# Performance work log

Hardware: AMD Instinct MI355X
Metric: run time of the kernel (lower is better)

Reference implementation:

```python
import math
import jax, jax.numpy as jnp
from jax import lax
import numpy as np

B, DIM, H, W = 8, 256, 64, 64
D_STATE, D_CONV, EXPAND = 16, 4, 2
D_INNER = EXPAND * DIM
DT_RANK = math.ceil(DIM / 16)
POS_LEN = 16
EPS = 1e-5
GN_GROUPS = 32


def setup_inputs() -> dict:
    key = jax.random.key(0)
    ks = iter(jax.random.split(key, 24))
    rn = lambda shape, s=0.02: jax.random.normal(next(ks), shape, jnp.float32) * s
    inp = {}
    inp["x"] = jax.random.normal(next(ks), (B, DIM, H, W), jnp.float32)
    inp["pos_emb"] = rn((1, DIM, POS_LEN), 1.0)
    inp["ln_g"] = jnp.ones((DIM,), jnp.float32)
    inp["ln_b"] = jnp.zeros((DIM,), jnp.float32)
    inp["m_in_w"] = rn((2, 2 * D_INNER, DIM))
    inp["m_conv_w"] = rn((2, D_INNER, D_CONV), 0.1)
    inp["m_conv_b"] = jnp.zeros((2, D_INNER), jnp.float32)
    inp["m_xproj_w"] = rn((2, DT_RANK + 2 * D_STATE, D_INNER))
    inp["m_dt_w"] = rn((2, D_INNER, DT_RANK), 0.1)
    inp["m_dt_b"] = rn((2, D_INNER), 0.1)
    inp["m_A_log"] = jnp.tile(jnp.log(jnp.arange(1, D_STATE + 1, dtype=jnp.float32))[None, None, :], (2, D_INNER, 1))
    inp["m_D"] = jnp.ones((2, D_INNER), jnp.float32)
    inp["m_out_w"] = rn((2, DIM, D_INNER))
    inp["proj_w"] = rn((DIM, 2 * DIM))
    inp["proj_b"] = jnp.zeros((DIM,), jnp.float32)
    inp["up_dw_w"] = rn((DIM, 1, 3, 3), 0.1)
    inp["up_bn1_g"] = jnp.ones((DIM,), jnp.float32)
    inp["up_bn1_b"] = jnp.zeros((DIM,), jnp.float32)
    inp["up_pw_w"] = rn((DIM, DIM), 0.05)
    inp["up_bn2_g"] = jnp.ones((DIM,), jnp.float32)
    inp["up_bn2_b"] = jnp.zeros((DIM,), jnp.float32)
    inp["down_pw_w"] = rn((DIM, DIM), 0.05)
    inp["down_bn_g"] = jnp.ones((DIM,), jnp.float32)
    inp["down_bn_b"] = jnp.zeros((DIM,), jnp.float32)
    inp["gn_g"] = jnp.ones((DIM,), jnp.float32)
    inp["gn_b"] = jnp.zeros((DIM,), jnp.float32)
    return inp


def reference(x, pos_emb, ln_g, ln_b, m_in_w, m_conv_w, m_conv_b, m_xproj_w, m_dt_w, m_dt_b,
              m_A_log, m_D, m_out_w, proj_w, proj_b, up_dw_w, up_bn1_g, up_bn1_b, up_pw_w,
              up_bn2_g, up_bn2_b, down_pw_w, down_bn_g, down_bn_b, gn_g, gn_b):
    Bx, C, Hh, Ww = x.shape

    def ln(t):  # LayerNorm over last dim (shared self.norm)
        m = jnp.mean(t, -1, keepdims=True)
        v = jnp.mean((t - m) ** 2, -1, keepdims=True)
        return (t - m) * lax.rsqrt(v + EPS) * ln_g + ln_b

    def bn(t, g, b):  # BatchNorm2d in eval mode with default running stats (mean 0, var 1)
        return t * (g / jnp.sqrt(1.0 + EPS))[None, :, None, None] + b[None, :, None, None]

    def gn(t):  # GroupNorm(32, C), shared params (self.bn)
        Bn, Cn, Hn, Wn = t.shape
        tg = t.reshape(Bn, GN_GROUPS, Cn // GN_GROUPS, Hn, Wn)
        m = jnp.mean(tg, (2, 3, 4), keepdims=True)
        v = jnp.mean((tg - m) ** 2, (2, 3, 4), keepdims=True)
        tg = (tg - m) * lax.rsqrt(v + EPS)
        return tg.reshape(Bn, Cn, Hn, Wn) * gn_g[None, :, None, None] + gn_b[None, :, None, None]

    def interp_pos(N):  # F.interpolate(pos_embed, size=N, mode='linear', align_corners=False)
        coords = jnp.maximum((jnp.arange(N, dtype=jnp.float32) + 0.5) * (POS_LEN / N) - 0.5, 0.0)
        i0 = jnp.floor(coords).astype(jnp.int32)
        i1 = jnp.minimum(i0 + 1, POS_LEN - 1)
        wgt = coords - i0.astype(jnp.float32)
        return pos_emb[:, :, i0] * (1.0 - wgt) + pos_emb[:, :, i1] * wgt  # (1,C,N)

    def pe_branch(vals, idx, N):  # vals (B,C,N); indices interp at same size = identity
        t = vals + interp_pos(N) + idx.astype(jnp.float32)
        return ln(jnp.swapaxes(t, 1, 2))  # (B,N,C)

    def mamba(u, d):  # standard mamba_ssm selective scan; u (B,L,C)
        xz = jnp.einsum('blc,ic->bli', u, m_in_w[d])
        xh, zg = jnp.split(xz, 2, -1)
        xc = lax.conv_general_dilated(jnp.swapaxes(xh, 1, 2), m_conv_w[d][:, None, :], (1,),
                                      [(D_CONV - 1, 0)], feature_group_count=D_INNER,
                                      dimension_numbers=('NCH', 'OIH', 'NCH'))
        xc = jnp.swapaxes(jax.nn.silu(xc + m_conv_b[d][None, :, None]), 1, 2)  # (B,L,di)
        dbl = jnp.einsum('bld,ed->ble', xc, m_xproj_w[d])
        dt = dbl[..., :DT_RANK]
        Bm = dbl[..., DT_RANK:DT_RANK + D_STATE]
        Cm = dbl[..., DT_RANK + D_STATE:]
        dt = jax.nn.softplus(jnp.einsum('blr,dr->bld', dt, m_dt_w[d]) + m_dt_b[d])  # (B,L,di)
        A = -jnp.exp(m_A_log[d])  # (di,ds)
        dA = jnp.exp(dt[..., None] * A)  # (B,L,di,ds)
        dBx = dt[..., None] * Bm[:, :, None, :] * xc[..., None]

        def step(h, inps):
            dA_t, dBx_t, C_t = inps
            h = dA_t * h + dBx_t
            return h, jnp.einsum('bds,bs->bd', h, C_t)

        h0 = jnp.zeros((u.shape[0], D_INNER, D_STATE), u.dtype)
        _, ys = lax.scan(step, h0, (jnp.swapaxes(dA, 0, 1), jnp.swapaxes(dBx, 0, 1), jnp.swapaxes(Cm, 0, 1)))
        y = jnp.swapaxes(ys, 0, 1) + xc * m_D[d]
        y = y * jax.nn.silu(zg)
        return jnp.einsum('bld,od->blo', y, m_out_w[d])

    # z branch: depthwise ConvTranspose2d(k3,s2,p1,op1) + BN + ReLU + pw conv + BN, then ReLU6
    z = lax.conv_general_dilated(x, jnp.flip(up_dw_w, (2, 3)), (1, 1), [(1, 2), (1, 2)],
                                 lhs_dilation=(2, 2), feature_group_count=C,
                                 dimension_numbers=('NCHW', 'OIHW', 'NCHW'))  # (B,C,2H,2W)
    z = jax.nn.relu(bn(z, up_bn1_g, up_bn1_b))
    z = jnp.einsum('bchw,oc->bohw', z, up_pw_w)
    z = jnp.clip(bn(z, up_bn2_g, up_bn2_b), 0.0, 6.0)

    col_max = pe_branch(jnp.max(x, 2), jnp.argmax(x, 2), Ww)
    col_min = pe_branch(jnp.min(x, 2), jnp.argmin(x, 2), Ww)
    row_max = pe_branch(jnp.max(x, 3), jnp.argmax(x, 3), Hh)
    row_min = pe_branch(jnp.min(x, 3), jnp.argmin(x, 3), Hh)
    result_max = jnp.concatenate([col_max, row_max], 1)  # (B, W+H, C)
    result_min = jnp.concatenate([col_min, row_min], 1)

    fm_max = ln(mamba(result_max, 0))
    fm_min = ln(mamba(result_min, 0))
    bm_max = ln(mamba(jnp.flip(result_max, 1), 1))
    bm_min = ln(mamba(jnp.flip(result_min, 1), 1))

    res_max = jnp.concatenate([fm_max, jnp.flip(bm_max, 1)], -1) @ proj_w.T + proj_b
    res_min = jnp.concatenate([fm_min, jnp.flip(bm_min, 1)], -1) @ proj_w.T + proj_b
    res_max = ln(res_max)[:, :, None, :]  # (B,L,1,C)
    res_min = ln(res_min)[:, None, :, :]  # (B,1,L,C)

    res = jnp.transpose(res_max + res_min, (0, 3, 1, 2))  # (B,C,L,L), L=H+W=2H
    res = jnp.clip(res + 3.0, 0.0, 6.0) / 6.0 * z  # h_sigmoid gate
    res = gn(res)
    res = jnp.einsum('bchw,oc->bohw', res[:, :, ::2, ::2], down_pw_w)  # pw conv stride 2
    res = bn(res, down_bn_g, down_bn_b)
    res = gn(res)
    res = res + x
    res = gn(res)
    return res
```

## Files before the change

kernel.cpp:

```cpp
#include <hip/hip_runtime.h>
#include <hip/hip_bf16.h>
#include <math.h>

typedef __hip_bfloat16 bf16;
typedef __attribute__((ext_vector_type(8))) short short8_t;
typedef __attribute__((ext_vector_type(4))) short short4_t;
typedef __attribute__((ext_vector_type(4))) float f32x4_t;

#define EPSV 1e-5f
#define BNSC 0.99999500003749968f

__device__ __forceinline__ float bf2f(bf16 v){ return __bfloat162float(v); }
__device__ __forceinline__ bf16 f2bf(float v){ return __float2bfloat16(v); }

__device__ __forceinline__ float blk_sum(float v, float* sm){
  int tid = threadIdx.x;
  #pragma unroll
  for(int o=32;o>0;o>>=1) v += __shfl_down(v, o, 64);
  if((tid&63)==0) sm[tid>>6] = v;
  __syncthreads();
  float s = 0.f;
  int nw = blockDim.x>>6;
  for(int i=0;i<nw;i++) s += sm[i];
  __syncthreads();
  return s;
}

__device__ __forceinline__ float softplusf(float x){
  return (x > 20.f) ? x : __logf(1.f + __expf(x));
}
__device__ __forceinline__ float siluf(float x){
  return x / (1.f + __expf(-x));
}

__global__ void prep_weights(const float* __restrict__ in_w, const float* __restrict__ out_w,
                             const float* __restrict__ pw_w, const float* __restrict__ dpw_w,
                             const float* __restrict__ proj_w,
                             bf16* __restrict__ Winb, bf16* __restrict__ Woutb,
                             bf16* __restrict__ Wub, bf16* __restrict__ Wdb,
                             float* __restrict__ PT, float* __restrict__ gacc){
  int idx = blockIdx.x*256 + threadIdx.x;
  if(idx < 1536) gacc[idx] = 0.f;
  if(idx < 524288){ Winb[idx] = f2bf(in_w[idx]); return; }
  if(idx < 786432){ int i=idx-524288; Woutb[i] = f2bf(out_w[i]); return; }
  if(idx < 851968){ int i=idx-786432; Wub[i] = f2bf(pw_w[i]); return; }
  if(idx < 917504){ int i=idx-851968; Wdb[i] = f2bf(dpw_w[i]); return; }
  int k = idx - 917504;
  int i = k >> 9, j = k & 511;
  PT[j*256 + i] = proj_w[k];
}

__global__ void r1_reduce_pe(const float* __restrict__ x, const float* __restrict__ pe,
                             float* __restrict__ pmax, float* __restrict__ pmin){
  __shared__ float tile[64*65];
  int bc = blockIdx.x;
  int b = bc >> 8, c = bc & 255;
  const float* xp = x + ((size_t)bc << 12);
  for(int i=threadIdx.x; i<4096; i+=64)
    tile[(i>>6)*65 + (i&63)] = xp[i];
  __syncthreads();
  int t = threadIdx.x;
  float cmx=-3.4e38f, cmn=3.4e38f; int cax=0, can=0;
  for(int h=0;h<64;h++){
    float v = tile[h*65 + t];
    if(v > cmx){ cmx=v; cax=h; }
    if(v < cmn){ cmn=v; can=h; }
  }
  float rmx=-3.4e38f, rmn=3.4e38f; int rax=0, ran=0;
  for(int w=0;w<64;w++){
    float v = tile[t*65 + w];
    if(v > rmx){ rmx=v; rax=w; }
    if(v < rmn){ rmn=v; ran=w; }
  }
  float coords = fmaxf((t + 0.5f)*0.25f - 0.5f, 0.f);
  int i0 = (int)floorf(coords);
  int i1 = min(i0+1, 15);
  float wg = coords - (float)i0;
  float pos = pe[c*16+i0]*(1.f-wg) + pe[c*16+i1]*wg;
  size_t base_col = ((size_t)b*128 + t)*256 + c;
  size_t base_row = ((size_t)b*128 + 64 + t)*256 + c;
  pmax[base_col] = cmx + pos + (float)cax;
  pmin[base_col] = cmn + pos + (float)can;
  pmax[base_row] = rmx + pos + (float)rax;
  pmin[base_row] = rmn + pos + (float)ran;
}

__global__ void ln_rows2(float* __restrict__ bufA, float* __restrict__ bufB,
                         const float* __restrict__ g, const float* __restrict__ bb,
                         bf16* __restrict__ boutA, bf16* __restrict__ boutB){
  __shared__ float sm[8];
  int row = blockIdx.x, t = threadIdx.x;
  float* buf; bf16* bout;
  if(row < 1024){ buf = bufA; bout = boutA; }
  else { buf = bufB; bout = boutB; row -= 1024; }
  float v = buf[(size_t)row*256 + t];
  float m = blk_sum(v, sm) * (1.f/256.f);
  float dv = v - m;
  float var = blk_sum(dv*dv, sm) * (1.f/256.f);
  float r = dv * rsqrtf(var + EPSV) * g[t] + bb[t];
  buf[(size_t)row*256 + t] = r;
  if(bout) bout[(size_t)row*256 + t] = f2bf(r);
}

__global__ __launch_bounds__(256,2)
void m1_mfma(const bf16* __restrict__ ubmax, const bf16* __restrict__ ubmin,
             const bf16* __restrict__ Win, float* __restrict__ xz){
  __shared__ bf16 att[64*264];
  int bx = blockIdx.x;
  int it = bx & 3, lt = (bx>>2)&1, b = (bx>>3)&7, r = bx>>6;
  int d = r & 1;
  const bf16* u = (r < 2) ? ubmax : ubmin;
  int flip = r & 1;
  int t = threadIdx.x;
  {
    int pr = t>>5, cc = (t&31)*8;
    #pragma unroll
    for(int i=0;i<8;i++){
      int p = pr + i*8;
      int l = lt*64 + p;
      int le = flip ? (127 - l) : l;
      short8_t v = *(const short8_t*)((const short*)u + ((size_t)(b*128 + le))*256 + cc);
      *(short8_t*)&att[p*264 + cc] = v;
    }
  }
  __syncthreads();
  int wv = t>>6, lane = t&63, quad = lane>>4, l16 = lane&15;
  int m0 = wv*64;
  f32x4_t acc[4][4];
  #pragma unroll
  for(int ms=0;ms<4;ms++)
    #pragma unroll
    for(int ns=0;ns<4;ns++) acc[ms][ns] = (f32x4_t){0.f,0.f,0.f,0.f};
  const short* wbase = (const short*)Win + ((size_t)d*1024 + it*256)*256;
  for(int k0=0;k0<256;k0+=32){
    short8_t afr[4], bfr[4];
    #pragma unroll
    for(int ms=0;ms<4;ms++)
      afr[ms] = *(const short8_t*)(wbase + (size_t)(m0 + ms*16 + l16)*256 + k0 + quad*8);
    #pragma unroll
    for(int ns=0;ns<4;ns++)
      bfr[ns] = *(const short8_t*)&att[(ns*16 + l16)*264 + k0 + quad*8];
    #pragma unroll
    for(int ms=0;ms<4;ms++)
      #pragma unroll
      for(int ns=0;ns<4;ns++)
        acc[ms][ns] = __builtin_amdgcn_mfma_f32_16x16x32_bf16(afr[ms], bfr[ns], acc[ms][ns], 0,0,0);
  }
  int rb = r*8 + b;
  #pragma unroll
  for(int ns=0;ns<4;ns++){
    int l = lt*64 + ns*16 + l16;
    float* dst = xz + ((size_t)rb*128 + l)*1024 + it*256;
    #pragma unroll
    for(int ms=0;ms<4;ms++){
      int i = m0 + ms*16 + quad*4;
      *(f32x4_t*)(dst + i) = acc[ms][ns];
    }
  }
}

__global__ __launch_bounds__(256)
void m234(const float* __restrict__ xz, const float* __restrict__ cw,
          const float* __restrict__ cb, const float* __restrict__ xproj,
          const float* __restrict__ dtw, const float* __restrict__ dtbias,
          float* __restrict__ xc, float* __restrict__ dbl, float* __restrict__ dt){
  __shared__ float xzs[4*512];
  __shared__ float xcs[512];
  __shared__ float pbuf[192];
  __shared__ float dblrow[48];
  int rowid = blockIdx.x;
  int rb = rowid >> 7, l = rowid & 127;
  int d = (rb >> 3) & 1;
  int t = threadIdx.x;
  #pragma unroll
  for(int i=0;i<8;i++){
    int idx = t + i*256;
    int r = idx >> 9, dd = idx & 511;
    int ls = l - 3 + r;
    xzs[idx] = (ls >= 0) ? xz[((size_t)rb*128 + ls)*1024 + dd] : 0.f;
  }
  __syncthreads();
  #pragma unroll
  for(int i=0;i<2;i++){
    int dd = t + i*256;
    const float* w = cw + (size_t)(d*512 + dd)*4;
    float s = cb[d*512 + dd];
    #pragma unroll
    for(int k=0;k<4;k++) s += xzs[k*512 + dd] * w[k];
    s = siluf(s);
    xcs[dd] = s;
    xc[(size_t)rowid*512 + dd] = s;
  }
  __syncthreads();
  if(t < 192){
    int e = t >> 2, part = t & 3;
    const float* wp = xproj + (size_t)(d*48 + e)*512 + part*128;
    const float* xr = xcs + part*128;
    float s = 0.f;
    for(int k=0;k<128;k++) s += xr[k]*wp[k];
    pbuf[t] = s;
  }
  __syncthreads();
  if(t < 48){
    float s = pbuf[t*4] + pbuf[t*4+1] + pbuf[t*4+2] + pbuf[t*4+3];
    dblrow[t] = s;
    dbl[(size_t)rowid*48 + t] = s;
  }
  __syncthreads();
  #pragma unroll
  for(int i=0;i<2;i++){
    int dd = t + i*256;
    const float* wp = dtw + (size_t)(d*512 + dd)*16;
    float s = dtbias[d*512 + dd];
    #pragma unroll
    for(int r=0;r<16;r++) s += dblrow[r]*wp[r];
    dt[(size_t)rowid*512 + dd] = softplusf(s);
  }
}

__global__ void m5_passA(const float* __restrict__ dt, const float* __restrict__ xc,
                         const float* __restrict__ dbl, const float* __restrict__ Alog,
                         float* __restrict__ P, float* __restrict__ Hl){
  int bx = blockIdx.x;
  int seg = bx & 7, half = (bx>>3)&1, rb = bx>>4;
  int dd = half*256 + threadIdx.x;
  int d = (rb>>3)&1;
  float A[16], h[16], pr[16];
  #pragma unroll
  for(int s=0;s<16;s++){
    A[s] = -__expf(Alog[(size_t)(d*512 + dd)*16 + s]);
    h[s] = 0.f; pr[s] = 1.f;
  }
  int l0 = seg*16;
  for(int l=l0;l<l0+16;l++){
    size_t row = (size_t)rb*128 + l;
    float dtv = dt[row*512 + dd];
    float xcv = xc[row*512 + dd];
    float bx_ = dtv*xcv;
    const float* dr = dbl + row*48;
    #pragma unroll
    for(int s=0;s<16;s++){
      float dA = __expf(dtv*A[s]);
      pr[s] *= dA;
      h[s] = dA*h[s] + bx_*dr[16+s];
    }
  }
  size_t o = ((size_t)(rb*8 + seg)*512 + dd)*16;
  #pragma unroll
  for(int s=0;s<16;s+=4){
    *(f32x4_t*)(P  + o + s) = (f32x4_t){pr[s],pr[s+1],pr[s+2],pr[s+3]};
    *(f32x4_t*)(Hl + o + s) = (f32x4_t){h[s],h[s+1],h[s+2],h[s+3]};
  }
}

__global__ void m5_passB(const float* __restrict__ dt, const float* __restrict__ xc,
                         const float* __restrict__ dbl, const float* __restrict__ xz,
                         const float* __restrict__ Alog, const float* __restrict__ Dp,
                         const float* __restrict__ P, const float* __restrict__ Hl,
                         bf16* __restrict__ ybb){
  int bx = blockIdx.x;
  int seg = bx & 7, half = (bx>>3)&1, rb = bx>>4;
  int dd = half*256 + threadIdx.x;
  int d = (rb>>3)&1;
  float A[16], h[16];
  #pragma unroll
  for(int s=0;s<16;s++){
    A[s] = -__expf(Alog[(size_t)(d*512 + dd)*16 + s]);
    h[s] = 0.f;
  }
  for(int j=0;j<seg;j++){
    size_t o = ((size_t)(rb*8 + j)*512 + dd)*16;
    #pragma unroll
    for(int s=0;s<16;s+=4){
      f32x4_t pv = *(const f32x4_t*)(P + o + s);
      f32x4_t hv = *(const f32x4_t*)(Hl + o + s);
      h[s]   = pv[0]*h[s]   + hv[0];
      h[s+1] = pv[1]*h[s+1] + hv[1];
      h[s+2] = pv[2]*h[s+2] + hv[2];
      h[s+3] = pv[3]*h[s+3] + hv[3];
    }
  }
  float Dv = Dp[d*512 + dd];
  int l0 = seg*16;
  for(int l=l0;l<l0+16;l++){
    size_t row = (size_t)rb*128 + l;
    float dtv = dt[row*512 + dd];
    float xcv = xc[row*512 + dd];
    float zgv = xz[row*1024 + 512 + dd];
    const float* dr = dbl + row*48;
    float bx_ = dtv*xcv;
    float y = 0.f;
    #pragma unroll
    for(int s=0;s<16;s++){
      h[s] = __expf(dtv*A[s])*h[s] + bx_*dr[16+s];
      y += h[s]*dr[32+s];
    }
    ybb[row*512 + dd] = f2bf((y + xcv*Dv) * siluf(zgv));
  }
}

__global__ __launch_bounds__(256,2)
void m6_mfma(const bf16* __restrict__ ybb, const bf16* __restrict__ Wout,
             const float* __restrict__ lng, const float* __restrict__ lnb,
             float* __restrict__ mo){
  __shared__ char smem[64*264*4];
  bf16* ybt = (bf16*)smem;
  float* fbuf = (float*)smem;
  int bx = blockIdx.x;
  int lt = bx & 1, b = (bx>>1)&7, r = bx>>4;
  int d = r & 1, rb = r*8 + b;
  size_t rowbase = (size_t)rb*128 + lt*64;
  int t = threadIdx.x;
  for(int i=t;i<4096;i+=256){
    int row = i>>6, c8 = (i&63)*8;
    short8_t v = *(const short8_t*)((const short*)ybb + (rowbase + row)*512 + c8);
    *(short8_t*)&ybt[row*520 + c8] = v;
  }
  __syncthreads();
  int wv = t>>6, lane = t&63, quad = lane>>4, l16 = lane&15;
  int m0 = wv*64;
  f32x4_t acc[4][4];
  #pragma unroll
  for(int ms=0;ms<4;ms++)
    #pragma unroll
    for(int ns=0;ns<4;ns++) acc[ms][ns] = (f32x4_t){0.f,0.f,0.f,0.f};
  const short* wbase = (const short*)Wout + (size_t)d*256*512;
  for(int k0=0;k0<512;k0+=32){
    short8_t afr[4], bfr[4];
    #pragma unroll
    for(int ms=0;ms<4;ms++)
      afr[ms] = *(const short8_t*)(wbase + (size_t)(m0 + ms*16 + l16)*512 + k0 + quad*8);
    #pragma unroll
    for(int ns=0;ns<4;ns++)
      bfr[ns] = *(const short8_t*)&ybt[(ns*16 + l16)*520 + k0 + quad*8];
    #pragma unroll
    for(int ms=0;ms<4;ms++)
      #pragma unroll
      for(int ns=0;ns<4;ns++)
        acc[ms][ns] = __builtin_amdgcn_mfma_f32_16x16x32_bf16(afr[ms], bfr[ns], acc[ms][ns], 0,0,0);
  }
  __syncthreads();
  #pragma unroll
  for(int ns=0;ns<4;ns++){
    int row = ns*16 + l16;
    #pragma unroll
    for(int ms=0;ms<4;ms++){
      int o = m0 + ms*16 + quad*4;
      *(f32x4_t*)(fbuf + row*264 + o) = acc[ms][ns];
    }
  }
  __syncthreads();
  {
    int row = t >> 2, part = t & 3;
    const float* fr = fbuf + row*264;
    float s = 0.f;
    #pragma unroll 8
    for(int j=0;j<64;j++){
      int col = part*64 + ((j + part*16) & 63);
      s += fr[col];
    }
    s += __shfl_xor(s, 1, 64);
    s += __shfl_xor(s, 2, 64);
    float m = s * (1.f/256.f);
    float q = 0.f;
    #pragma unroll 8
    for(int j=0;j<64;j++){
      int col = part*64 + ((j + part*16) & 63);
      float dv = fr[col] - m;
      q += dv*dv;
    }
    q += __shfl_xor(q, 1, 64);
    q += __shfl_xor(q, 2, 64);
    float rs = rsqrtf(q*(1.f/256.f) + EPSV);
    float* dst = mo + (rowbase + row)*256;
    for(int j=0;j<64;j++){
      int col = part*64 + j;
      dst[col] = (fr[col] - m)*rs*lng[col] + lnb[col];
    }
  }
}

__global__ void m7_proj(const float* __restrict__ mo, const float* __restrict__ PT,
                        const float* __restrict__ pb, const float* __restrict__ lng,
                        const float* __restrict__ lnb, float* __restrict__ resm,
                        float* __restrict__ resn){
  __shared__ float ct[16*512];
  __shared__ float fbuf[16*264];
  int bx = blockIdx.x;
  int tt = bx >> 6, rem = bx & 63, b = rem >> 3, lt = rem & 7;
  int fr_ = tt*2, br = tt*2 + 1;
  for(int i=threadIdx.x;i<16*512;i+=256){
    int lr = i >> 9, k = i & 511;
    int l = lt*16 + lr;
    ct[i] = (k < 256)
      ? mo[(((size_t)(fr_*8+b)*128) + l)*256 + k]
      : mo[(((size_t)(br*8+b)*128) + (127-l))*256 + (k-256)];
  }
  __syncthreads();
  float acc[16];
  #pragma unroll
  for(int q=0;q<16;q++) acc[q] = 0.f;
  int t = threadIdx.x;
  for(int k=0;k<512;k++){
    float pv = PT[(size_t)k*256 + t];
    #pragma unroll
    for(int q=0;q<16;q++) acc[q] += pv * ct[(q<<9) + k];
  }
  float bias = pb[t];
  #pragma unroll
  for(int q=0;q<16;q++) fbuf[q*264 + t] = acc[q] + bias;
  __syncthreads();
  float* dstbuf = tt ? resn : resm;
  if(t < 64){
    int row = t >> 2, part = t & 3;
    const float* fr = fbuf + row*264;
    float s = 0.f;
    for(int j=0;j<64;j++){
      int col = part*64 + ((j + part*16) & 63);
      s += fr[col];
    }
    s += __shfl_xor(s, 1, 64);
    s += __shfl_xor(s, 2, 64);
    float m = s * (1.f/256.f);
    float q = 0.f;
    for(int j=0;j<64;j++){
      int col = part*64 + ((j + part*16) & 63);
      float dv = fr[col] - m;
      q += dv*dv;
    }
    q += __shfl_xor(q, 1, 64);
    q += __shfl_xor(q, 2, 64);
    float rs = rsqrtf(q*(1.f/256.f) + EPSV);
    float* dst = dstbuf + ((size_t)b*128 + lt*16 + row)*256;
    for(int j=0;j<64;j++){
      int col = part*64 + j;
      dst[col] = (fr[col] - m)*rs*lng[col] + lnb[col];
    }
  }
}

__global__ __launch_bounds__(256)
void k1_deconv_T(const float* __restrict__ x, const float* __restrict__ wdw,
                 const float* __restrict__ g1, const float* __restrict__ b1,
                 bf16* __restrict__ zT){
  __shared__ float in[2*64*33];
  __shared__ bf16 ot[64*80];
  int bx = blockIdx.x;
  int cb = bx & 3, half = (bx>>2)&1, h = (bx>>3)&127, b = bx>>10;
  int c0 = cb*64, w0 = half*64, iw0 = w0>>1;
  int h_odd = h & 1;
  int ihA = h_odd ? (h-1)>>1 : h>>1;
  int ihB = (h+1)>>1;
  bool hasB = h_odd && (ihB < 64);
  for(int i = threadIdx.x; i < 4224; i += 256){
    int row = i / 2112;
    int rem = i - row*2112;
    int c = rem / 33;
    int iw = rem - c*33;
    int ihl = row ? ihB : ihA;
    bool valid = (iw0 + iw < 64) && (row == 0 || hasB);
    in[i] = valid ? x[(((size_t)b*256 + c0 + c)<<12) + (ihl<<6) + iw0 + iw] : 0.f;
  }
  __syncthreads();
  int c = threadIdx.x & 63, g = threadIdx.x >> 6;
  const float* wp = wdw + (c0+c)*9;
  int khA3 = h_odd ? 6 : 3;
  float wA0 = wp[khA3], wA1 = wp[khA3+1], wA2 = wp[khA3+2];
  float wB0 = wp[0],    wB1 = wp[1],      wB2 = wp[2];
  float scale = g1[c0+c]*BNSC, bias = b1[c0+c];
  const float* inA = in + c*33;
  const float* inB = in + 2112 + c*33;
  #pragma unroll
  for(int i=0;i<16;i++){
    int wi = g*16 + i;
    float s;
    if(!(i&1)){
      int iw = wi>>1;
      s = inA[iw]*wA1 + inB[iw]*wB1;
    } else {
      int iwa = (wi-1)>>1, iwb = (wi+1)>>1;
      s = inA[iwa]*wA2 + inA[iwb]*wA0 + inB[iwa]*wB2 + inB[iwb]*wB0;
    }
    ot[wi*80 + c] = f2bf(fmaxf(s*scale + bias, 0.f));
  }
  __syncthreads();
  int rr = threadIdx.x >> 3;
  int co = (threadIdx.x & 7) * 8;
  size_t obase = (((size_t)b*16384) + (size_t)h*128 + w0)*256 + c0;
  #pragma unroll
  for(int pass=0; pass<2; pass++){
    int wi = rr + pass*32;
    short8_t v = *(const short8_t*)&ot[wi*80 + co];
    *(short8_t*)((short*)zT + obase + (size_t)wi*256 + co) = v;
  }
}

__global__ __launch_bounds__(256,2)
void k2_mfma(const bf16* __restrict__ zT, const bf16* __restrict__ Wub,
             const float* __restrict__ g2, const float* __restrict__ b2,
             const float* __restrict__ resm, const float* __restrict__ resn,
             bf16* __restrict__ resT, float* __restrict__ gsum, float* __restrict__ gssq){
  __shared__ bf16 zt[128*264];
  __shared__ float lsum[32], lssq[32];
  int b = blockIdx.y;
  int p0 = blockIdx.x*128;
  int t = threadIdx.x;
  if(t < 32){ lsum[t] = 0.f; lssq[t] = 0.f; }
  {
    const short* src = (const short*)zT + (((size_t)b*16384 + p0)*256);
    int pr = t>>5;
    int cc = (t&31)*8;
    #pragma unroll
    for(int i=0;i<16;i++){
      int p = pr + i*8;
      short8_t v = *(const short8_t*)(src + (size_t)p*256 + cc);
      *(short8_t*)&zt[p*264 + cc] = v;
    }
  }
  __syncthreads();
  int wv = t>>6, lane = t&63, quad = lane>>4, l16 = lane&15;
  int m0 = wv*64;
  f32x4_t acc[4][8];
  #pragma unroll
  for(int ms=0;ms<4;ms++)
    #pragma unroll
    for(int ns=0;ns<8;ns++) acc[ms][ns] = (f32x4_t){0.f,0.f,0.f,0.f};
  const short* wp = (const short*)Wub + (size_t)(m0 + l16)*256 + quad*8;
  short8_t afr[4];
  #pragma unroll
  for(int ms=0;ms<4;ms++) afr[ms] = *(const short8_t*)(wp + (size_t)ms*16*256);
  for(int k0=0;k0<256;k0+=32){
    short8_t anext[4];
    if(k0 + 32 < 256){
      #pragma unroll
      for(int ms=0;ms<4;ms++)
        anext[ms] = *(const short8_t*)(wp + (size_t)ms*16*256 + k0 + 32);
    }
    short8_t bfr[8];
    #pragma unroll
    for(int ns=0;ns<8;ns++)
      bfr[ns] = *(const short8_t*)&zt[(ns*16 + l16)*264 + k0 + quad*8];
    #pragma unroll
    for(int ms=0;ms<4;ms++)
      #pragma unroll
      for(int ns=0;ns<8;ns++)
        acc[ms][ns] = __builtin_amdgcn_mfma_f32_16x16x32_bf16(afr[ms], bfr[ns], acc[ms][ns], 0,0,0);
    #pragma unroll
    for(int ms=0;ms<4;ms++) afr[ms] = anext[ms];
  }
  float sm_[4] = {0.f,0.f,0.f,0.f}, sq_[4] = {0.f,0.f,0.f,0.f};
  #pragma unroll
  for(int ns=0;ns<8;ns++){
    int p = p0 + ns*16 + l16;
    int hh = p>>7, ww = p&127;
    const float* rm = resm + ((size_t)b*128+hh)*256;
    const float* rn = resn + ((size_t)b*128+ww)*256;
    size_t orow = ((size_t)b*16384 + p)*256;
    #pragma unroll
    for(int ms=0;ms<4;ms++){
      int o = m0 + ms*16 + quad*4;
      f32x4_t a = acc[ms][ns];
      f32x4_t gv = *(const f32x4_t*)(g2+o);
      f32x4_t bv = *(const f32x4_t*)(b2+o);
      f32x4_t rmv = *(const f32x4_t*)(rm+o);
      f32x4_t rnv = *(const f32x4_t*)(rn+o);
      alignas(8) bf16 ov[4];
      #pragma unroll
      for(int r=0;r<4;r++){
        float zv = a[r]*(gv[r]*BNSC) + bv[r];
        zv = fminf(fmaxf(zv, 0.f), 6.f);
        float gate = fminf(fmaxf(rmv[r]+rnv[r]+3.f, 0.f), 6.f)*(1.f/6.f);
        float val = zv*gate;
        sm_[ms] += val;
        sq_[ms] += val*val;
        ov[r] = f2bf(val);
      }
      *(short4_t*)((short*)resT + orow + o) = *(const short4_t*)ov;
    }
  }
  #pragma unroll
  for(int ms=0;ms<4;ms++){
    int g = ((m0 + ms*16) >> 3) + (quad >> 1);
    atomicAdd(&lsum[g], sm_[ms]);
    atomicAdd(&lssq[g], sq_[ms]);
  }
  __syncthreads();
  if(t < 32){
    atomicAdd(&gsum[b*32 + t], lsum[t]);
    atomicAdd(&gssq[b*32 + t], lssq[t]);
  }
}

__global__ __launch_bounds__(256,2)
void k4_mfma(const bf16* __restrict__ resT, const bf16* __restrict__ Wdb,
             const float* __restrict__ gsum1, const float* __restrict__ gssq1,
             const float* __restrict__ gng, const float* __restrict__ gnb,
             const float* __restrict__ dbg, const float* __restrict__ dbb,
             float* __restrict__ t1, float* __restrict__ gsum2, float* __restrict__ gssq2){
  __shared__ bf16 at[64*264];
  __shared__ float sc[256], sb[256];
  __shared__ float stm[32], str[32];
  __shared__ float l2s[32], l2q[32];
  int b = blockIdx.y;
  int q0 = blockIdx.x*64;
  int t = threadIdx.x;
  if(t < 32){
    l2s[t] = 0.f; l2q[t] = 0.f;
    float m = gsum1[b*32+t] * (1.f/131072.f);
    float var = gssq1[b*32+t] * (1.f/131072.f) - m*m;
    stm[t] = m;
    str[t] = rsqrtf(var + EPSV);
  }
  __syncthreads();
  {
    int cch = t, g = cch>>3;
    float m = stm[g], rs = str[g];
    float s = rs*gng[cch];
    sc[cch] = s; sb[cch] = gnb[cch] - m*s;
  }
  __syncthreads();
  {
    int pr = t>>5;
    int cc = (t&31)*8;
    #pragma unroll
    for(int i=0;i<8;i++){
      int q = pr + i*8;
      int qq = q0 + q;
      int y = qq>>6, xw = qq&63;
      size_t srow = ((size_t)b*16384 + (size_t)y*256 + xw*2)*256;
      short8_t v = *(const short8_t*)((const short*)resT + srow + cc);
      const bf16* vv = (const bf16*)&v;
      alignas(16) bf16 ov[8];
      #pragma unroll
      for(int j=0;j<8;j++) ov[j] = f2bf(bf2f(vv[j])*sc[cc+j] + sb[cc+j]);
      *(short8_t*)&at[q*264 + cc] = *(const short8_t*)ov;
    }
  }
  __syncthreads();
  int wv = t>>6, lane = t&63, quad = lane>>4, l16 = lane&15;
  int n0 = wv*64;
  f32x4_t acc[4][4];
  #pragma unroll
  for(int ms=0;ms<4;ms++)
    #pragma unroll
    for(int ns=0;ns<4;ns++) acc[ms][ns] = (f32x4_t){0.f,0.f,0.f,0.f};
  for(int k0=0;k0<256;k0+=32){
    short8_t afr[4], bfr[4];
    #pragma unroll
    for(int ms=0;ms<4;ms++) afr[ms] = *(const short8_t*)&at[(ms*16 + l16)*264 + k0 + quad*8];
    const short* wp = (const short*)Wdb + (size_t)(n0 + l16)*256 + k0 + quad*8;
    #pragma unroll
    for(int ns=0;ns<4;ns++) bfr[ns] = *(const short8_t*)(wp + (size_t)ns*16*256);
    #pragma unroll
    for(int ms=0;ms<4;ms++)
      #pragma unroll
      for(int ns=0;ns<4;ns++)
        acc[ms][ns] = __builtin_amdgcn_mfma_f32_16x16x32_bf16(afr[ms], bfr[ns], acc[ms][ns], 0,0,0);
  }
  #pragma unroll
  for(int ns=0;ns<4;ns++){
    int o = n0 + ns*16 + l16;
    float s2 = dbg[o]*BNSC, bb2 = dbb[o];
    float* dst = t1 + (((size_t)b*256 + o) << 12);
    float s_=0.f, q_=0.f;
    #pragma unroll
    for(int ms=0;ms<4;ms++){
      int ps = q0 + ms*16 + quad*4;
      f32x4_t a = acc[ms][ns];
      f32x4_t ov;
      #pragma unroll
      for(int r=0;r<4;r++){
        ov[r] = a[r]*s2 + bb2;
        s_ += ov[r];
        q_ += ov[r]*ov[r];
      }
      *(f32x4_t*)(dst + ps) = ov;
    }
    atomicAdd(&l2s[o>>3], s_);
    atomicAdd(&l2q[o>>3], q_);
  }
  __syncthreads();
  if(t < 32){
    atomicAdd(&gsum2[b*32 + t], l2s[t]);
    atomicAdd(&gssq2[b*32 + t], l2q[t]);
  }
}

__global__ void k6_gn_add(float* __restrict__ t1, const float* __restrict__ x,
                          const float* __restrict__ gsum2, const float* __restrict__ gssq2,
                          const float* __restrict__ gng, const float* __restrict__ gnb,
                          float* __restrict__ gsum3, float* __restrict__ gssq3){
  __shared__ float sm[8];
  int i4 = blockIdx.x*256 + threadIdx.x;
  int idx = i4 << 2;
  int c = (idx >> 12) & 255, b = idx >> 20, g = c >> 3;
  float m2 = gsum2[b*32+g] * (1.f/32768.f);
  float var = gssq2[b*32+g] * (1.f/32768.f) - m2*m2;
  float rs = rsqrtf(var + EPSV);
  float scl = rs*gng[c], off = gnb[c] - m2*scl;
  f32x4_t tv = *(const f32x4_t*)(t1 + idx);
  f32x4_t xv = *(const f32x4_t*)(x + idx);
  f32x4_t ov;
  float S = 0.f, Q = 0.f;
  #pragma unroll
  for(int r=0;r<4;r++){
    float v = tv[r]*scl + off + xv[r];
    ov[r] = v;
    S += v; Q += v*v;
  }
  *(f32x4_t*)(t1 + idx) = ov;
  S = blk_sum(S, sm);
  Q = blk_sum(Q, sm);
  if(threadIdx.x == 0){
    atomicAdd(&gsum3[b*32 + g], S);
    atomicAdd(&gssq3[b*32 + g], Q);
  }
}

__global__ void k8_gn_out(const float* __restrict__ t1, const float* __restrict__ gsum3,
                          const float* __restrict__ gssq3, const float* __restrict__ gng,
                          const float* __restrict__ gnb, float* __restrict__ out){
  int i4 = blockIdx.x*256 + threadIdx.x;
  int idx = i4 << 2;
  int c = (idx >> 12) & 255, b = idx >> 20, g = c >> 3;
  float m = gsum3[b*32+g] * (1.f/32768.f);
  float var = gssq3[b*32+g] * (1.f/32768.f) - m*m;
  float rs = rsqrtf(var + EPSV);
  float scl = rs*gng[c], off = gnb[c] - m*scl;
  f32x4_t tv = *(const f32x4_t*)(t1 + idx);
  f32x4_t ov;
  #pragma unroll
  for(int r=0;r<4;r++) ov[r] = tv[r]*scl + off;
  *(f32x4_t*)(out + idx) = ov;
}

extern "C" void kernel_launch(void* const* d_in, const int* in_sizes, int n_in,
                              void* d_out, int out_size, void* d_ws, size_t ws_size,
                              hipStream_t stream){
  const float* x      = (const float*)d_in[0];
  const float* pos    = (const float*)d_in[1];
  const float* ln_g   = (const float*)d_in[2];
  const float* ln_b   = (const float*)d_in[3];
  const float* in_w   = (const float*)d_in[4];
  const float* conv_w = (const float*)d_in[5];
  const float* conv_b = (const float*)d_in[6];
  const float* xproj  = (const float*)d_in[7];
  const float* dt_w   = (const float*)d_in[8];
  const float* dt_b   = (const float*)d_in[9];
  const float* A_log  = (const float*)d_in[10];
  const float* Dp     = (const float*)d_in[11];
  const float* out_w  = (const float*)d_in[12];
  const float* proj_w = (const float*)d_in[13];
  const float* proj_b = (const float*)d_in[14];
  const float* dw_w   = (const float*)d_in[15];
  const float* bn1g   = (const float*)d_in[16];
  const float* bn1b   = (const float*)d_in[17];
  const float* pw_w   = (const float*)d_in[18];
  const float* bn2g   = (const float*)d_in[19];
  const float* bn2b   = (const float*)d_in[20];
  const float* dpw_w  = (const float*)d_in[21];
  const float* dbng   = (const float*)d_in[22];
  const float* dbnb   = (const float*)d_in[23];
  const float* gng    = (const float*)d_in[24];
  const float* gnb    = (const float*)d_in[25];
  float* out = (float*)d_out;

  float* ws = (float*)d_ws;
  bf16*  resT = (bf16*)ws;
  bf16*  zT   = (bf16*)(ws + 16777216);
  float* scanP = ws + 16777216;
  float* scanH = ws + 16777216 + 2097152;
  float* zone = ws + 33554432;
  float* xz   = zone;
  float* xc   = xz  + 4194304;
  float* dbl  = xc  + 2097152;
  float* dtb  = dbl + 196608;
  bf16*  ybb  = (bf16*)(dtb + 2097152);
  float* t1   = zone;
  float* mo   = zone + 9633792;
  float* resm = mo   + 1048576;
  float* resn = resm + 262144;
  float* pmax = resn + 262144;
  float* pmin = pmax + 262144;
  float* PT   = pmin + 262144;
  bf16*  ubmax= (bf16*)(PT + 131072);
  bf16*  ubmin= (bf16*)(PT + 131072 + 131072);
  bf16*  Winb = (bf16*)(PT + 131072 + 262144);
  bf16*  Woutb= (bf16*)(PT + 131072 + 524288);
  bf16*  Wub  = (bf16*)(PT + 131072 + 655360);
  bf16*  Wdb  = (bf16*)(PT + 131072 + 688128);
  float* gacc = PT + 131072 + 720896;
  float* gsum1 = gacc,        *gssq1 = gacc + 256;
  float* gsum2 = gacc + 512,  *gssq2 = gacc + 768;
  float* gsum3 = gacc + 1024, *gssq3 = gacc + 1280;

  prep_weights<<<4096,256,0,stream>>>(in_w, out_w, pw_w, dpw_w, proj_w,
                                      Winb, Woutb, Wub, Wdb, PT, gacc);

  r1_reduce_pe<<<2048,64,0,stream>>>(x, pos, pmax, pmin);
  ln_rows2<<<2048,256,0,stream>>>(pmax, pmin, ln_g, ln_b, ubmax, ubmin);

  m1_mfma<<<256,256,0,stream>>>(ubmax, ubmin, Winb, xz);
  m234<<<4096,256,0,stream>>>(xz, conv_w, conv_b, xproj, dt_w, dt_b, xc, dbl, dtb);
  m5_passA<<<512,256,0,stream>>>(dtb, xc, dbl, A_log, scanP, scanH);
  m5_passB<<<512,256,0,stream>>>(dtb, xc, dbl, xz, A_log, Dp, scanP, scanH, ybb);
  m6_mfma<<<64,256,0,stream>>>(ybb, Woutb, ln_g, ln_b, mo);
  m7_proj<<<128,256,0,stream>>>(mo, PT, proj_b, ln_g, ln_b, resm, resn);

  k1_deconv_T<<<8192,256,0,stream>>>(x, dw_w, bn1g, bn1b, zT);
  k2_mfma<<<dim3(128,8),256,0,stream>>>(zT, Wub, bn2g, bn2b, resm, resn,
                                        resT, gsum1, gssq1);

  k4_mfma<<<dim3(64,8),256,0,stream>>>(resT, Wdb, gsum1, gssq1,
                                       gng, gnb, dbng, dbnb, t1, gsum2, gssq2);

  k6_gn_add<<<8192,256,0,stream>>>(t1, x, gsum2, gssq2, gng, gnb, gsum3, gssq3);
  k8_gn_out<<<8192,256,0,stream>>>(t1, gsum3, gssq3, gng, gnb, out);
}
```

Before: 527.1 us.

## Enlarge k4 tile, prefetch weights, replace LDS atomics with wave shuffle reductions

In k2 and k4 the group-norm statistics are now summed with cross-lane shuffles and written to global memory with direct atomics, which removes the shared-memory atomics and a block barrier. k4 now processes 128 output positions per block instead of 64, which halves the grid and reuses each loaded weight fragment across twice as many MFMAs. It also prefetches the next k-step's weight fragments into registers. The larger accumulator array raises register pressure and the larger LDS tile can lower occupancy, and the global atomics now come from more threads.

Result: slower. 553.1 us (+4.9%).

```diff
diff --git a/kernel.cpp b/kernel.cpp
--- a/kernel.cpp
+++ b/kernel.cpp
@@ -501,11 +501,9 @@
              const float* __restrict__ resm, const float* __restrict__ resn,
              bf16* __restrict__ resT, float* __restrict__ gsum, float* __restrict__ gssq){
   __shared__ bf16 zt[128*264];
-  __shared__ float lsum[32], lssq[32];
   int b = blockIdx.y;
   int p0 = blockIdx.x*128;
   int t = threadIdx.x;
-  if(t < 32){ lsum[t] = 0.f; lssq[t] = 0.f; }
   {
     const short* src = (const short*)zT + (((size_t)b*16384 + p0)*256);
     int pr = t>>5;
@@ -580,14 +578,17 @@
   }
   #pragma unroll
   for(int ms=0;ms<4;ms++){
-    int g = ((m0 + ms*16) >> 3) + (quad >> 1);
-    atomicAdd(&lsum[g], sm_[ms]);
-    atomicAdd(&lssq[g], sq_[ms]);
-  }
-  __syncthreads();
-  if(t < 32){
-    atomicAdd(&gsum[b*32 + t], lsum[t]);
-    atomicAdd(&gssq[b*32 + t], lssq[t]);
+    float S = sm_[ms], Q = sq_[ms];
+    #pragma unroll
+    for(int o=1;o<=16;o<<=1){
+      S += __shfl_xor(S, o, 32);
+      Q += __shfl_xor(Q, o, 32);
+    }
+    if((lane & 31) == 0){
+      int g = ((m0 + ms*16) >> 3) + (quad >> 1);
+      atomicAdd(&gsum[b*32 + g], S);
+      atomicAdd(&gssq[b*32 + g], Q);
+    }
   }
 }
 
@@ -597,15 +598,13 @@
              const float* __restrict__ gng, const float* __restrict__ gnb,
              const float* __restrict__ dbg, const float* __restrict__ dbb,
              float* __restrict__ t1, float* __restrict__ gsum2, float* __restrict__ gssq2){
-  __shared__ bf16 at[64*264];
+  __shared__ bf16 at[128*264];
   __shared__ float sc[256], sb[256];
   __shared__ float stm[32], str[32];
-  __shared__ float l2s[32], l2q[32];
   int b = blockIdx.y;
-  int q0 = blockIdx.x*64;
+  int q0 = blockIdx.x*128;
   int t = threadIdx.x;
   if(t < 32){
-    l2s[t] = 0.f; l2q[t] = 0.f;
     float m = gsum1[b*32+t] * (1.f/131072.f);
     float var = gssq1[b*32+t] * (1.f/131072.f) - m*m;
     stm[t] = m;
@@ -623,7 +622,7 @@
     int pr = t>>5;
     int cc = (t&31)*8;
     #pragma unroll
-    for(int i=0;i<8;i++){
+    for(int i=0;i<16;i++){
       int q = pr + i*8;
       int qq = q0 + q;
       int y = qq>>6, xw = qq&63;
@@ -639,23 +638,33 @@
   __syncthreads();
   int wv = t>>6, lane = t&63, quad = lane>>4, l16 = lane&15;
   int n0 = wv*64;
-  f32x4_t acc[4][4];
-  #pragma unroll
-  for(int ms=0;ms<4;ms++)
+  f32x4_t acc[8][4];
+  #pragma unroll
+  for(int ms=0;ms<8;ms++)
     #pragma unroll
     for(int ns=0;ns<4;ns++) acc[ms][ns] = (f32x4_t){0.f,0.f,0.f,0.f};
+  const short* wp = (const short*)Wdb + (size_t)(n0 + l16)*256 + quad*8;
+  short8_t bfr[4];
+  #pragma unroll
+  for(int ns=0;ns<4;ns++) bfr[ns] = *(const short8_t*)(wp + (size_t)ns*16*256);
   for(int k0=0;k0<256;k0+=32){
-    short8_t afr[4], bfr[4];
-    #pragma unroll
-    for(int ms=0;ms<4;ms++) afr[ms] = *(const short8_t*)&at[(ms*16 + l16)*264 + k0 + quad*8];
-    const short* wp = (const short*)Wdb + (size_t)(n0 + l16)*256 + k0 + quad*8;
-    #pragma unroll
-    for(int ns=0;ns<4;ns++) bfr[ns] = *(const short8_t*)(wp + (size_t)ns*16*256);
-    #pragma unroll
-    for(int ms=0;ms<4;ms++)
+    short8_t bnext[4];
+    if(k0 + 32 < 256){
+      #pragma unroll
+      for(int ns=0;ns<4;ns++)
+        bnext[ns] = *(const short8_t*)(wp + (size_t)ns*16*256 + k0 + 32);
+    }
+    short8_t afr[8];
+    #pragma unroll
+    for(int ms=0;ms<8;ms++)
+      afr[ms] = *(const short8_t*)&at[(ms*16 + l16)*264 + k0 + quad*8];
+    #pragma unroll
+    for(int ms=0;ms<8;ms++)
       #pragma unroll
       for(int ns=0;ns<4;ns++)
         acc[ms][ns] = __builtin_amdgcn_mfma_f32_16x16x32_bf16(afr[ms], bfr[ns], acc[ms][ns], 0,0,0);
+    #pragma unroll
+    for(int ns=0;ns<4;ns++) bfr[ns] = bnext[ns];
   }
   #pragma unroll
   for(int ns=0;ns<4;ns++){
@@ -664,7 +673,7 @@
     float* dst = t1 + (((size_t)b*256 + o) << 12);
     float s_=0.f, q_=0.f;
     #pragma unroll
-    for(int ms=0;ms<4;ms++){
+    for(int ms=0;ms<8;ms++){
       int ps = q0 + ms*16 + quad*4;
       f32x4_t a = acc[ms][ns];
       f32x4_t ov;
@@ -676,13 +685,19 @@
       }
       *(f32x4_t*)(dst + ps) = ov;
     }
-    atomicAdd(&l2s[o>>3], s_);
-    atomicAdd(&l2q[o>>3], q_);
-  }
-  __syncthreads();
-  if(t < 32){
-    atomicAdd(&gsum2[b*32 + t], l2s[t]);
-    atomicAdd(&gssq2[b*32 + t], l2q[t]);
+    #pragma unroll
+    for(int msk=1; msk<=4; msk<<=1){
+      s_ += __shfl_xor(s_, msk, 64);
+      q_ += __shfl_xor(q_, msk, 64);
+    }
+    s_ += __shfl_xor(s_, 16, 64);
+    q_ += __shfl_xor(q_, 16, 64);
+    s_ += __shfl_xor(s_, 32, 64);
+    q_ += __shfl_xor(q_, 32, 64);
+    if(((l16 & 7) == 0) && (quad == 0)){
+      atomicAdd(&gsum2[b*32 + (o>>3)], s_);
+      atomicAdd(&gssq2[b*32 + (o>>3)], q_);
+    }
   }
 }
 
@@ -811,7 +826,7 @@
   k2_mfma<<<dim3(128,8),256,0,stream>>>(zT, Wub, bn2g, bn2b, resm, resn,
                                         resT, gsum1, gssq1);
 
-  k4_mfma<<<dim3(64,8),256,0,stream>>>(resT, Wdb, gsum1, gssq1,
+  k4_mfma<<<dim3(32,8),256,0,stream>>>(resT, Wdb, gsum1, gssq1,
                                        gng, gnb, dbng, dbnb, t1, gsum2, gssq2);
 
   k6_gn_add<<<8192,256,0,stream>>>(t1, x, gsum2, gssq2, gng, gnb, gsum3, gssq3);
```
